# Kernel tuning notes

Hardware: AMD Instinct MI355X
Metric: run time of the kernel (lower is better)

Reference implementation:

```python
import jax, jax.numpy as jnp
import numpy as np

N_NODES = 50000
N_EDGES = 800000
H = 64  # n_hid


def _linear_params(key, fan_in, fan_out):
    lim = 1.0 / np.sqrt(fan_in)
    kw, kb = jax.random.split(key)
    w = jax.random.uniform(kw, (fan_in, fan_out), minval=-lim, maxval=lim, dtype=jnp.float32)
    b = jax.random.uniform(kb, (fan_out,), minval=-lim, maxval=lim, dtype=jnp.float32)
    return w, b


def setup_inputs() -> dict:
    key = jax.random.key(0)
    ks = jax.random.split(key, 10)
    nf_gc = jax.random.normal(ks[0], (N_NODES, H), dtype=jnp.float32)
    src = jax.random.randint(ks[1], (N_EDGES,), 0, N_NODES, dtype=jnp.int32)
    dst = jax.random.randint(ks[2], (N_EDGES,), 0, N_NODES, dtype=jnp.int32)
    res_w1, res_b1 = _linear_params(ks[3], H, H)
    res_w2, res_b2 = _linear_params(ks[4], H, H)
    lin1_w, lin1_b = _linear_params(ks[5], H, H)
    lin2_w, lin2_b = _linear_params(ks[6], H, H)
    msg_w1, msg_b1 = _linear_params(ks[7], 2 * H, 2 * H)
    msg_w2, msg_b2 = _linear_params(ks[8], 2 * H, 2 * H + 1)
    red_w, red_b = _linear_params(ks[9], 3 * H, H)
    return {
        'nf_gc': nf_gc, 'src': src, 'dst': dst,
        'res_w1': res_w1, 'res_b1': res_b1, 'res_w2': res_w2, 'res_b2': res_b2,
        'lin1_w': lin1_w, 'lin1_b': lin1_b, 'lin2_w': lin2_w, 'lin2_b': lin2_b,
        'msg_w1': msg_w1, 'msg_b1': msg_b1, 'msg_w2': msg_w2, 'msg_b2': msg_b2,
        'red_w': red_w, 'red_b': red_b,
    }


def reference(nf_gc, src, dst, res_w1, res_b1, res_w2, res_b2,
              lin1_w, lin1_b, lin2_w, lin2_b,
              msg_w1, msg_b1, msg_w2, msg_b2, red_w, red_b):
    n = nf_gc.shape[0]
    h = lin1_w.shape[0]
    # Residual block: lin2(lin1(x)) + x (no activation)
    x = ((nf_gc @ res_w1 + res_b1) @ res_w2 + res_b2) + nf_gc
    x1 = x @ lin1_w + lin1_b
    # Edge message: concat(src feat, dst feat) -> MLP(2h -> 2h -> 2h+1)
    e = jnp.concatenate([x[src], x[dst]], axis=1)          # [E, 2h]
    hmid = jax.nn.leaky_relu(e @ msg_w1 + msg_b1, 0.2)     # [E, 2h]
    o = hmid @ msg_w2 + msg_b2                             # [E, 2h+1]
    k = jax.nn.sigmoid(o[:, :1])
    f1 = o[:, 1:1 + h] * k
    f2 = o[:, 1 + h:] * k
    # Scatter-reduce: sum for f1, max for f2 (DGL gives 0 for isolated nodes)
    nfoc1 = jax.ops.segment_sum(f1, dst, num_segments=n)
    neg_inf = jnp.array(-jnp.inf, dtype=f2.dtype)
    nfoc2 = jnp.full((n, h), neg_inf, dtype=f2.dtype).at[dst].max(f2)
    deg = jnp.zeros((n,), dtype=f2.dtype).at[dst].add(1.0)
    nfoc2 = jnp.where(deg[:, None] > 0, nfoc2, 0.0)
    # Node reduce MLP (single linear 3h -> h), then outer lin2
    new_x = jnp.concatenate([x, nfoc1, nfoc2], axis=1) @ red_w + red_b
    x2 = new_x @ lin2_w + lin2_b
    return x1 + x2
```

## Files before the change

kernel.cpp:

```cpp
#include <hip/hip_runtime.h>

#define NN 50000
#define NE 800000

typedef _Float16 half8 __attribute__((ext_vector_type(8)));
typedef _Float16 half4 __attribute__((ext_vector_type(4)));
typedef _Float16 half2v __attribute__((ext_vector_type(2)));
typedef float f32x4 __attribute__((ext_vector_type(4)));
typedef unsigned long long u64;

static const size_t XHOFF  = 0;
static const size_t POFF   = 3200000;
static const size_t QOFF   = 6400000;
static const size_t N1OFF  = 9600000;
static const size_t N2OFF  = 12800000;
static const size_t W2TOFF = 16000000;
static const size_t WGHOFF = 16008192;
static const size_t RW1HOFF= 16008256;
static const size_t RW2HOFF= 16010304;
static const size_t L1WHOFF= 16012352;
static const size_t PWHOFF = 16014400;
static const size_t QWHOFF = 16018496;
static const size_t CNTOFF = 16022592;
static const size_t CUROFF = 16072592;
static const size_t PARTOFF= 16122592;
static const size_t SDOFF  = 16122848;
static const size_t FWOFF  = 17722848;
static const size_t FBOFF  = 17729200;

__device__ __forceinline__ unsigned fenc(float f){
  unsigned b = __float_as_uint(f);
  return (b & 0x80000000u) ? ~b : (b | 0x80000000u);
}
__device__ __forceinline__ float fdec(unsigned u){
  return (u & 0x80000000u) ? __uint_as_float(u & 0x7fffffffu) : __uint_as_float(~u);
}

__device__ __forceinline__ int kperm(int kp){
  const int kg = kp >> 5, rem = kp & 31, kt = rem >> 2, j = rem & 3;
  return kt*16 + kg*4 + j;
}

__global__ __launch_bounds__(256) void prep_k(
    const float* __restrict__ w2, const float* __restrict__ rw1,
    const float* __restrict__ rw2, const float* __restrict__ l1w,
    const float* __restrict__ mw1,
    const float* __restrict__ redw, const float* __restrict__ redb,
    const float* __restrict__ l2w, const float* __restrict__ l2b,
    _Float16* __restrict__ w2t, _Float16* __restrict__ w2gh,
    _Float16* __restrict__ rw1h, _Float16* __restrict__ rw2h,
    _Float16* __restrict__ l1wh, _Float16* __restrict__ pwh,
    _Float16* __restrict__ qwh,
    _Float16* __restrict__ fwh, float* __restrict__ fb,
    uint4* __restrict__ nfz,
    const int* __restrict__ dst, unsigned* __restrict__ counts)
{
  __shared__ float sl2[64][8];
  const int b = blockIdx.x;
  if (b < 177){
    int i = b * 256 + threadIdx.x;
    if (i < 16384){
      int c = i >> 7, kp = i & 127;
      w2t[i] = (_Float16)w2[kperm(kp)*129 + 1 + c];
    } else if (i < 16512){
      int kp = i - 16384;
      w2gh[kp] = (_Float16)w2[kperm(kp)*129];
    } else if (i < 20608){
      int idx = i - 16512, c = idx >> 6, k = idx & 63;
      rw1h[idx] = (_Float16)rw1[k*64 + c];
    } else if (i < 24704){
      int idx = i - 20608, c = idx >> 6, k = idx & 63;
      rw2h[idx] = (_Float16)rw2[k*64 + c];
    } else if (i < 28800){
      int idx = i - 24704, c = idx >> 6, k = idx & 63;
      l1wh[idx] = (_Float16)l1w[k*64 + c];
    } else if (i < 36992){
      int idx = i - 28800, c = idx >> 6, k = idx & 63;
      pwh[idx] = (_Float16)mw1[k*128 + c];
    } else if (i < 45184){
      int idx = i - 36992, c = idx >> 6, k = idx & 63;
      qwh[idx] = (_Float16)mw1[(64 + k)*128 + c];
    }
  } else if (b < 185){
    const int b2 = b - 177;
    const int c0 = b2 * 8;
    const int t = threadIdx.x;
    #pragma unroll
    for (int i = 0; i < 2; ++i){
      int idx = t + i*256;
      int j = idx >> 3, cc = idx & 7;
      sl2[j][cc] = l2w[j*64 + c0 + cc];
    }
    __syncthreads();
    for (int o = t; o < 1536; o += 256){
      int k = o >> 3, cc = o & 7;
      const float4* rw = (const float4*)&redw[k*64];
      float a = 0.f;
      #pragma unroll
      for (int q = 0; q < 16; ++q){
        const float4 r4 = rw[q];
        a = fmaf(r4.x, sl2[q*4+0][cc], a);
        a = fmaf(r4.y, sl2[q*4+1][cc], a);
        a = fmaf(r4.z, sl2[q*4+2][cc], a);
        a = fmaf(r4.w, sl2[q*4+3][cc], a);
      }
      fwh[(size_t)(c0 + cc)*192 + k] = (_Float16)a;
    }
    if (t < 8){
      float a = l2b[c0 + t];
      #pragma unroll 8
      for (int j = 0; j < 64; ++j) a = fmaf(redb[j], sl2[j][t], a);
      fb[c0 + t] = a;
    }
  } else if (b < 1748){
    const size_t i0 = ((size_t)(b - 185) * 256 + threadIdx.x) * 4;
    #pragma unroll
    for (int i = 0; i < 4; ++i){
      const size_t idx = i0 + i;
      if (idx < 1600000) nfz[idx] = make_uint4(0u,0u,0u,0u);
    }
  } else {
    int e = (b - 1748) * 256 + threadIdx.x;
    if (e < NE) atomicAdd(&counts[dst[e]], 1u);
  }
}

__global__ __launch_bounds__(256) void scanA(const unsigned* __restrict__ counts,
                                             unsigned* __restrict__ partial)
{
  __shared__ unsigned s[256];
  const int t = threadIdx.x;
  const int idx = blockIdx.x * 256 + t;
  s[t] = (idx < NN) ? counts[idx] : 0u;
  __syncthreads();
  for (int d = 128; d > 0; d >>= 1){
    if (t < d) s[t] += s[t + d];
    __syncthreads();
  }
  if (t == 0) partial[blockIdx.x] = s[0];
}

__global__ __launch_bounds__(256) void scanC2(const unsigned* __restrict__ counts,
                                              const unsigned* __restrict__ partial,
                                              unsigned* __restrict__ cursor)
{
  __shared__ unsigned sp[256];
  __shared__ unsigned s[256];
  const int t = threadIdx.x;
  const int b = blockIdx.x;
  sp[t] = (t < 196 && t < b) ? partial[t] : 0u;
  __syncthreads();
  for (int d = 128; d > 0; d >>= 1){
    if (t < d) sp[t] += sp[t + d];
    __syncthreads();
  }
  const unsigned boff = sp[0];
  const int idx = b * 256 + t;
  unsigned v = (idx < NN) ? counts[idx] : 0u;
  s[t] = v;
  __syncthreads();
  for (int d = 1; d < 256; d <<= 1){
    unsigned u = (t >= d) ? s[t - d] : 0u;
    __syncthreads();
    s[t] += u;
    __syncthreads();
  }
  if (idx < NN) cursor[idx] = boff + s[t] - v;
}

__global__ __launch_bounds__(256) void combo_k(
    const int* __restrict__ src, const int* __restrict__ dst,
    unsigned* __restrict__ cursor, u64* __restrict__ sdbuf,
    const float* __restrict__ nf,
    const _Float16* __restrict__ rw1h, const float* __restrict__ rb1,
    const _Float16* __restrict__ rw2h, const float* __restrict__ rb2,
    const _Float16* __restrict__ l1wh, const float* __restrict__ l1b,
    const _Float16* __restrict__ pwh, const _Float16* __restrict__ qwh,
    const float* __restrict__ mb1,
    _Float16* __restrict__ xh, _Float16* __restrict__ Pp, _Float16* __restrict__ Qp,
    float* __restrict__ out)
{
  __shared__ _Float16 sM[64][72];
  __shared__ _Float16 sT[64][72];
  const int b = blockIdx.x;
  const int t = threadIdx.x;

  if (b < 3125){
    int e = b * 256 + t;
    if (e < NE){
      const int d = dst[e];
      unsigned slot = atomicAdd(&cursor[d], 1u);
      sdbuf[slot] = ((u64)(unsigned)d << 32) | (unsigned)src[e];
    }
    return;
  }

  const int lane = t & 63, wv = t >> 6;
  const int l15 = lane & 15, kg = lane >> 4;
  const int n0 = (b - 3125) * 64;

  {
    const int rr = t >> 4, c4 = (t & 15) * 4;
    #pragma unroll
    for (int i = 0; i < 4; ++i){
      int r = rr + i*16, n = n0 + r;
      float4 v = make_float4(0.f,0.f,0.f,0.f);
      if (n < NN) v = *(const float4*)&nf[(size_t)n*64 + c4];
      half4 h; h[0]=(_Float16)v.x; h[1]=(_Float16)v.y; h[2]=(_Float16)v.z; h[3]=(_Float16)v.w;
      *(half4*)&sM[r][c4] = h;
    }
  }
  __syncthreads();

  const int col = wv*16 + l15;

  {
    half4 bf[4];
    #pragma unroll
    for (int kt = 0; kt < 4; ++kt) bf[kt] = *(const half4*)&rw1h[col*64 + kt*16 + kg*4];
    const float bias = rb1[col];
    #pragma unroll
    for (int rt = 0; rt < 4; ++rt){
      f32x4 acc = {0.f,0.f,0.f,0.f};
      #pragma unroll
      for (int kt = 0; kt < 4; ++kt){
        const half4 af = *(const half4*)&sM[rt*16 + l15][kt*16 + kg*4];
        acc = __builtin_amdgcn_mfma_f32_16x16x16f16(af, bf[kt], acc, 0, 0, 0);
      }
      #pragma unroll
      for (int reg = 0; reg < 4; ++reg)
        sT[rt*16 + kg*4 + reg][col] = (_Float16)(acc[reg] + bias);
    }
  }
  __syncthreads();

  {
    half4 bf[4];
    #pragma unroll
    for (int kt = 0; kt < 4; ++kt) bf[kt] = *(const half4*)&rw2h[col*64 + kt*16 + kg*4];
    const float bias = rb2[col];
    #pragma unroll
    for (int rt = 0; rt < 4; ++rt){
      f32x4 acc = {0.f,0.f,0.f,0.f};
      #pragma unroll
      for (int kt = 0; kt < 4; ++kt){
        const half4 af = *(const half4*)&sT[rt*16 + l15][kt*16 + kg*4];
        acc = __builtin_amdgcn_mfma_f32_16x16x16f16(af, bf[kt], acc, 0, 0, 0);
      }
      #pragma unroll
      for (int reg = 0; reg < 4; ++reg){
        const int row = rt*16 + kg*4 + reg;
        const float xv = acc[reg] + bias + (float)sM[row][col];
        const _Float16 xvh = (_Float16)xv;
        const int n = n0 + row;
        if (n < NN) xh[(size_t)n*64 + col] = xvh;
        sM[row][col] = xvh;
      }
    }
  }
  __syncthreads();

  {
    half4 bf[4];
    #pragma unroll
    for (int kt = 0; kt < 4; ++kt) bf[kt] = *(const half4*)&l1wh[col*64 + kt*16 + kg*4];
    const float bias = l1b[col];
    #pragma unroll
    for (int rt = 0; rt < 4; ++rt){
      f32x4 acc = {0.f,0.f,0.f,0.f};
      #pragma unroll
      for (int kt = 0; kt < 4; ++kt){
        const half4 af = *(const half4*)&sM[rt*16 + l15][kt*16 + kg*4];
        acc = __builtin_amdgcn_mfma_f32_16x16x16f16(af, bf[kt], acc, 0, 0, 0);
      }
      #pragma unroll
      for (int reg = 0; reg < 4; ++reg){
        const int row = rt*16 + kg*4 + reg;
        const int n = n0 + row;
        if (n < NN) out[(size_t)n*64 + col] = acc[reg] + bias;
      }
    }
  }

  #pragma unroll
  for (int g = 0; g < 2; ++g){
    const _Float16* WH = g ? qwh : pwh;
    _Float16* dstp = g ? Qp : Pp;
    #pragma unroll
    for (int h = 0; h < 2; ++h){
      const int ct = h*4 + wv;
      const int colp = ct*16 + l15;
      half4 bf[4];
      #pragma unroll
      for (int kt = 0; kt < 4; ++kt) bf[kt] = *(const half4*)&WH[colp*64 + kt*16 + kg*4];
      const float bias = g ? 0.f : mb1[colp];
      const int kgc = l15 >> 2, jj = l15 & 3;
      const int pos = kgc*32 + ct*4 + jj;
      #pragma unroll
      for (int rt = 0; rt < 4; ++rt){
        f32x4 acc = {0.f,0.f,0.f,0.f};
        #pragma unroll
        for (int kt = 0; kt < 4; ++kt){
          const half4 af = *(const half4*)&sM[rt*16 + l15][kt*16 + kg*4];
          acc = __builtin_amdgcn_mfma_f32_16x16x16f16(af, bf[kt], acc, 0, 0, 0);
        }
        #pragma unroll
        for (int reg = 0; reg < 4; ++reg){
          const int row = rt*16 + kg*4 + reg;
          const int n = n0 + row;
          if (n < NN) dstp[(size_t)n*128 + pos] = (_Float16)(acc[reg] + bias);
        }
      }
    }
  }
}

__global__ __launch_bounds__(256) void edge_mlp11(
    const u64* __restrict__ sd,
    const _Float16* __restrict__ Pp, const _Float16* __restrict__ Qp,
    const _Float16* __restrict__ w2t, const _Float16* __restrict__ w2gh,
    const float* __restrict__ b2,
    float* __restrict__ nfoc1, unsigned* __restrict__ nfoc2)
{
  __shared__ _Float16 sA[64][132];
  __shared__ _Float16 sOutHh[64][68];
  __shared__ float sK[2][64];
  __shared__ int   sD[2][64];
  const int t = threadIdx.x;
  const int lane = t & 63, wv = t >> 6;
  const int r  = lane & 15;
  const int kg = lane >> 4;
  const int row0 = wv * 16;
  const int base = blockIdx.x * 256;

  half4 bf0[8], bf1[8];
  half8 wgr[4];
  float bias0, bias1;
  {
    const int col0 = wv*16 + r, col1 = (wv+4)*16 + r;
    bias0 = b2[1 + col0]; bias1 = b2[1 + col1];
    const _Float16* w0p = &w2t[(size_t)col0*128 + kg*32];
    const _Float16* w1p = &w2t[(size_t)col1*128 + kg*32];
    #pragma unroll
    for (int kt = 0; kt < 8; ++kt){
      bf0[kt] = *(const half4*)&w0p[kt*4];
      bf1[kt] = *(const half4*)&w1p[kt*4];
    }
    #pragma unroll
    for (int i = 0; i < 4; ++i) wgr[i] = *(const half8*)&w2gh[kg*32 + i*8];
  }
  const float gb = b2[0];

#if __has_builtin(__builtin_amdgcn_fdot2)
#define GATE_ACC(MV, WG, GP) { \
    _Pragma("unroll") \
    for (int jj_ = 0; jj_ < 4; ++jj_){ \
      half2v a_ = { MV[jj_*2], MV[jj_*2+1] }; \
      half2v b_ = { WG[jj_*2], WG[jj_*2+1] }; \
      GP = __builtin_amdgcn_fdot2(a_, b_, GP, false); \
    } }
#else
#define GATE_ACC(MV, WG, GP) { \
    _Pragma("unroll") \
    for (int jj_ = 0; jj_ < 8; ++jj_) \
      GP = fmaf((float)MV[jj_], (float)WG[jj_], GP); }
#endif

#define LOADRAW(PH, QH, SS, DD, TILE) { \
    const u64 sdv = sd[base + (TILE)*64 + row0 + r]; \
    SS = (int)(unsigned)(sdv & 0xffffffffu); \
    DD = (int)(unsigned)(sdv >> 32); \
    const _Float16* pr = &Pp[(size_t)SS * 128 + kg*32]; \
    const _Float16* qr = &Qp[(size_t)DD * 128 + kg*32]; \
    PH[0] = *(const half8*)&pr[0];  PH[1] = *(const half8*)&pr[8]; \
    PH[2] = *(const half8*)&pr[16]; PH[3] = *(const half8*)&pr[24]; \
    QH[0] = *(const half8*)&qr[0];  QH[1] = *(const half8*)&qr[8]; \
    QH[2] = *(const half8*)&qr[16]; QH[3] = *(const half8*)&qr[24]; }

#define PROCESS(PH, QH, DD, BUF) { \
    if (kg == 0) sD[BUF][row0 + r] = DD; \
    float gp = 0.f; \
    _Pragma("unroll") \
    for (int i = 0; i < 4; ++i){ \
      half8 mv = PH[i] + QH[i]; \
      const half8 m2 = mv * (_Float16)0.2f; \
      mv = __builtin_elementwise_max(mv, m2); \
      GATE_ACC(mv, wgr[i], gp); \
      *(half8*)&sA[row0 + r][kg*32 + i*8] = mv; \
    } \
    gp += __shfl_xor(gp, 16); \
    gp += __shfl_xor(gp, 32); \
    if (kg == 0) sK[BUF][row0 + r] = 1.f / (1.f + expf(-(gp + gb))); }

#define COMPUTE_HALF(BF, BIAS) { \
    _Pragma("unroll") \
    for (int rt = 0; rt < 4; ++rt){ \
      half4 af[8]; \
      const _Float16* ar = &sA[rt*16 + r][kg*32]; \
      _Pragma("unroll") \
      for (int kt = 0; kt < 8; ++kt) af[kt] = *(const half4*)&ar[kt*4]; \
      f32x4 a0 = {0.f,0.f,0.f,0.f}; \
      _Pragma("unroll") \
      for (int kt = 0; kt < 8; ++kt) \
        a0 = __builtin_amdgcn_mfma_f32_16x16x16f16(af[kt], BF[kt], a0, 0, 0, 0); \
      _Pragma("unroll") \
      for (int reg = 0; reg < 4; ++reg){ \
        const int row = rt*16 + kg*4 + reg; \
        sOutHh[row][wv*16 + r] = (_Float16)(a0[reg] + BIAS); \
      } \
    } }

#define REDUCE_SUM(BUF) { \
    const int c = t & 63; \
    const int rbeg = (t >> 6) * 16; \
    float acc = 0.f; \
    int curd = sD[BUF][rbeg]; \
    _Pragma("unroll 4") \
    for (int rw = rbeg; rw < rbeg + 16; ++rw){ \
      acc += (float)sOutHh[rw][c] * sK[BUF][rw]; \
      const bool last = (rw == rbeg + 15) || (sD[BUF][rw + 1] != curd); \
      if (last){ \
        unsafeAtomicAdd(&nfoc1[(size_t)curd*64 + c], acc); \
        acc = 0.f; \
        if (rw < rbeg + 15) curd = sD[BUF][rw + 1]; \
      } \
    } }

#define REDUCE_MAX(BUF) { \
    const int c = t & 63; \
    const int rbeg = (t >> 6) * 16; \
    float acc = -1e30f; \
    int curd = sD[BUF][rbeg]; \
    _Pragma("unroll 4") \
    for (int rw = rbeg; rw < rbeg + 16; ++rw){ \
      acc = fmaxf(acc, (float)sOutHh[rw][c] * sK[BUF][rw]); \
      const bool last = (rw == rbeg + 15) || (sD[BUF][rw + 1] != curd); \
      if (last){ \
        atomicMax(&nfoc2[(size_t)curd*64 + c], fenc(acc)); \
        acc = -1e30f; \
        if (rw < rbeg + 15) curd = sD[BUF][rw + 1]; \
      } \
    } }

#define TILE_BODY(BUF) \
    __syncthreads(); \
    COMPUTE_HALF(bf0, bias0); \
    __syncthreads(); \
    REDUCE_SUM(BUF); \
    __syncthreads(); \
    COMPUTE_HALF(bf1, bias1); \
    __syncthreads(); \
    REDUCE_MAX(BUF);

  int s0, d0, s1, d1;
  half8 ph0[4], qh0[4], ph1[4], qh1[4];

  LOADRAW(ph0, qh0, s0, d0, 0);

  LOADRAW(ph1, qh1, s1, d1, 1);
  PROCESS(ph0, qh0, d0, 0);
  TILE_BODY(0);

  LOADRAW(ph0, qh0, s0, d0, 2);
  PROCESS(ph1, qh1, d1, 1);
  TILE_BODY(1);

  LOADRAW(ph1, qh1, s1, d1, 3);
  PROCESS(ph0, qh0, d0, 0);
  TILE_BODY(0);

  PROCESS(ph1, qh1, d1, 1);
  TILE_BODY(1);

#undef LOADRAW
#undef PROCESS
#undef COMPUTE_HALF
#undef REDUCE_SUM
#undef REDUCE_MAX
#undef TILE_BODY
#undef GATE_ACC
}

__global__ __launch_bounds__(256) void node_post_m(
    const _Float16* __restrict__ xh, const float* __restrict__ nfoc1,
    const unsigned* __restrict__ nfoc2, const unsigned* __restrict__ counts,
    const _Float16* __restrict__ fwh, const float* __restrict__ fb,
    float* __restrict__ out)
{
  __shared__ _Float16 sC[64][200];
  const int t = threadIdx.x;
  const int lane = t & 63, wv = t >> 6;
  const int l15 = lane & 15, kg = lane >> 4;
  const int n0 = blockIdx.x * 64;

  {
    const int rr = t >> 4, c4 = (t & 15) * 4;
    #pragma unroll
    for (int i = 0; i < 4; ++i){
      int r = rr + i*16, n = n0 + r;
      half4 xv = {};
      float4 f1 = make_float4(0,0,0,0);
      uint4 f2 = make_uint4(0,0,0,0);
      bool has = false;
      if (n < NN){
        xv = *(const half4*)&xh[(size_t)n*64 + c4];
        f1 = *(const float4*)&nfoc1[(size_t)n*64 + c4];
        f2 = *(const uint4*)&nfoc2[(size_t)n*64 + c4];
        has = counts[n] > 0u;
      }
      *(half4*)&sC[r][c4] = xv;
      half4 h1; h1[0]=(_Float16)f1.x; h1[1]=(_Float16)f1.y; h1[2]=(_Float16)f1.z; h1[3]=(_Float16)f1.w;
      *(half4*)&sC[r][64 + c4] = h1;
      half4 h2;
      h2[0] = has ? (_Float16)fdec(f2.x) : (_Float16)0.f;
      h2[1] = has ? (_Float16)fdec(f2.y) : (_Float16)0.f;
      h2[2] = has ? (_Float16)fdec(f2.z) : (_Float16)0.f;
      h2[3] = has ? (_Float16)fdec(f2.w) : (_Float16)0.f;
      *(half4*)&sC[r][128 + c4] = h2;
    }
  }
  __syncthreads();

  const int col = wv*16 + l15;
  half4 bf[12];
  #pragma unroll
  for (int kt = 0; kt < 12; ++kt) bf[kt] = *(const half4*)&fwh[col*192 + kt*16 + kg*4];
  const float bias = fb[col];

  #pragma unroll
  for (int rt = 0; rt < 4; ++rt){
    f32x4 acc = {0.f,0.f,0.f,0.f};
    #pragma unroll
    for (int kt = 0; kt < 12; ++kt){
      const half4 af = *(const half4*)&sC[rt*16 + l15][kt*16 + kg*4];
      acc = __builtin_amdgcn_mfma_f32_16x16x16f16(af, bf[kt], acc, 0, 0, 0);
    }
    #pragma unroll
    for (int reg = 0; reg < 4; ++reg){
      const int row = rt*16 + kg*4 + reg;
      const int n = n0 + row;
      if (n < NN) out[(size_t)n*64 + col] += acc[reg] + bias;
    }
  }
}

extern "C" void kernel_launch(void* const* d_in, const int* in_sizes, int n_in,
                              void* d_out, int out_size, void* d_ws, size_t ws_size,
                              hipStream_t stream)
{
  const float* nf   = (const float*)d_in[0];
  const int*   src  = (const int*)d_in[1];
  const int*   dst  = (const int*)d_in[2];
  const float* rw1  = (const float*)d_in[3];
  const float* rb1  = (const float*)d_in[4];
  const float* rw2  = (const float*)d_in[5];
  const float* rb2  = (const float*)d_in[6];
  const float* l1w  = (const float*)d_in[7];
  const float* l1b  = (const float*)d_in[8];
  const float* l2w  = (const float*)d_in[9];
  const float* l2b  = (const float*)d_in[10];
  const float* mw1  = (const float*)d_in[11];
  const float* mb1  = (const float*)d_in[12];
  const float* mw2  = (const float*)d_in[13];
  const float* mb2  = (const float*)d_in[14];
  const float* redw = (const float*)d_in[15];
  const float* redb = (const float*)d_in[16];

  float* ws = (float*)d_ws;
  _Float16*  xh     = (_Float16*)(ws + XHOFF);
  _Float16*  P      = (_Float16*)(ws + POFF);
  _Float16*  Q      = (_Float16*)(ws + QOFF);
  float*     nfoc1  = ws + N1OFF;
  unsigned*  nfoc2  = (unsigned*)(ws + N2OFF);
  _Float16*  w2t    = (_Float16*)(ws + W2TOFF);
  _Float16*  w2gh   = (_Float16*)(ws + WGHOFF);
  _Float16*  rw1h   = (_Float16*)(ws + RW1HOFF);
  _Float16*  rw2h   = (_Float16*)(ws + RW2HOFF);
  _Float16*  l1wh   = (_Float16*)(ws + L1WHOFF);
  _Float16*  pwh    = (_Float16*)(ws + PWHOFF);
  _Float16*  qwh    = (_Float16*)(ws + QWHOFF);
  unsigned*  counts = (unsigned*)(ws + CNTOFF);
  unsigned*  cursor = (unsigned*)(ws + CUROFF);
  unsigned*  partial= (unsigned*)(ws + PARTOFF);
  u64*       sdbuf  = (u64*)(ws + SDOFF);
  _Float16*  fwh    = (_Float16*)(ws + FWOFF);
  float*     fb     = ws + FBOFF;
  float*     out    = (float*)d_out;

  hipMemsetAsync(counts, 0, NN * sizeof(unsigned), stream);
  hipLaunchKernelGGL(prep_k, dim3(1748 + 3125), dim3(256), 0, stream,
                     mw2, rw1, rw2, l1w, mw1, redw, redb, l2w, l2b,
                     w2t, w2gh, rw1h, rw2h, l1wh, pwh, qwh, fwh, fb,
                     (uint4*)nfoc1, dst, counts);
  hipLaunchKernelGGL(scanA, dim3(196), dim3(256), 0, stream, counts, partial);
  hipLaunchKernelGGL(scanC2, dim3(196), dim3(256), 0, stream, counts, partial, cursor);
  hipLaunchKernelGGL(combo_k, dim3(3125 + 782), dim3(256), 0, stream,
                     src, dst, cursor, sdbuf,
                     nf, rw1h, rb1, rw2h, rb2, l1wh, l1b, pwh, qwh, mb1,
                     xh, P, Q, out);
  hipLaunchKernelGGL(edge_mlp11, dim3(3125), dim3(256), 0, stream,
                     sdbuf, P, Q, w2t, w2gh, mb2, nfoc1, nfoc2);
  hipLaunchKernelGGL(node_post_m, dim3(782), dim3(256), 0, stream,
                     xh, nfoc1, nfoc2, counts, fwh, fb, out);
}
```

Before: 280.8 us.

## Merge scan kernels, move lin1 into node post, use lighter edge barriers

Replaces the two-kernel scan with a single kernel in which each block sums all preceding counts directly, removing one launch. The lin1 projection moves from combo_k into the node post kernel, where its MFMAs run on the x slice already staged in shared memory. This removes the write and read-modify-write of out in fp32. The edge kernel's __syncthreads are replaced by raw s_barrier plus an lgkmcnt wait and sched barriers, to cut barrier overhead. The trade-offs are redundant reads of counts in the scan (later blocks read up to about 50K values) and reliance on the vmcnt not needing a wait at those barriers.

```diff
diff --git a/kernel.cpp b/kernel.cpp
--- a/kernel.cpp
+++ b/kernel.cpp
@@ -23,7 +23,6 @@
 static const size_t QWHOFF = 16018496;
 static const size_t CNTOFF = 16022592;
 static const size_t CUROFF = 16072592;
-static const size_t PARTOFF= 16122592;
 static const size_t SDOFF  = 16122848;
 static const size_t FWOFF  = 17722848;
 static const size_t FBOFF  = 17729200;
@@ -125,30 +124,17 @@
   }
 }
 
-__global__ __launch_bounds__(256) void scanA(const unsigned* __restrict__ counts,
-                                             unsigned* __restrict__ partial)
-{
-  __shared__ unsigned s[256];
-  const int t = threadIdx.x;
-  const int idx = blockIdx.x * 256 + t;
-  s[t] = (idx < NN) ? counts[idx] : 0u;
-  __syncthreads();
-  for (int d = 128; d > 0; d >>= 1){
-    if (t < d) s[t] += s[t + d];
-    __syncthreads();
-  }
-  if (t == 0) partial[blockIdx.x] = s[0];
-}
-
-__global__ __launch_bounds__(256) void scanC2(const unsigned* __restrict__ counts,
-                                              const unsigned* __restrict__ partial,
+__global__ __launch_bounds__(256) void scanAC(const unsigned* __restrict__ counts,
                                               unsigned* __restrict__ cursor)
 {
   __shared__ unsigned sp[256];
   __shared__ unsigned s[256];
   const int t = threadIdx.x;
   const int b = blockIdx.x;
-  sp[t] = (t < 196 && t < b) ? partial[t] : 0u;
+  unsigned acc = 0;
+  const int lim = b * 256;
+  for (int i = t; i < lim; i += 256) acc += counts[i];
+  sp[t] = acc;
   __syncthreads();
   for (int d = 128; d > 0; d >>= 1){
     if (t < d) sp[t] += sp[t + d];
@@ -174,11 +160,9 @@
     const float* __restrict__ nf,
     const _Float16* __restrict__ rw1h, const float* __restrict__ rb1,
     const _Float16* __restrict__ rw2h, const float* __restrict__ rb2,
-    const _Float16* __restrict__ l1wh, const float* __restrict__ l1b,
     const _Float16* __restrict__ pwh, const _Float16* __restrict__ qwh,
     const float* __restrict__ mb1,
-    _Float16* __restrict__ xh, _Float16* __restrict__ Pp, _Float16* __restrict__ Qp,
-    float* __restrict__ out)
+    _Float16* __restrict__ xh, _Float16* __restrict__ Pp, _Float16* __restrict__ Qp)
 {
   __shared__ _Float16 sM[64][72];
   __shared__ _Float16 sT[64][72];
@@ -259,28 +243,6 @@
     }
   }
   __syncthreads();
-
-  {
-    half4 bf[4];
-    #pragma unroll
-    for (int kt = 0; kt < 4; ++kt) bf[kt] = *(const half4*)&l1wh[col*64 + kt*16 + kg*4];
-    const float bias = l1b[col];
-    #pragma unroll
-    for (int rt = 0; rt < 4; ++rt){
-      f32x4 acc = {0.f,0.f,0.f,0.f};
-      #pragma unroll
-      for (int kt = 0; kt < 4; ++kt){
-        const half4 af = *(const half4*)&sM[rt*16 + l15][kt*16 + kg*4];
-        acc = __builtin_amdgcn_mfma_f32_16x16x16f16(af, bf[kt], acc, 0, 0, 0);
-      }
-      #pragma unroll
-      for (int reg = 0; reg < 4; ++reg){
-        const int row = rt*16 + kg*4 + reg;
-        const int n = n0 + row;
-        if (n < NN) out[(size_t)n*64 + col] = acc[reg] + bias;
-      }
-    }
-  }
 
   #pragma unroll
   for (int g = 0; g < 2; ++g){
@@ -315,7 +277,7 @@
   }
 }
 
-__global__ __launch_bounds__(256) void edge_mlp11(
+__global__ __launch_bounds__(256) void edge_mlp12(
     const u64* __restrict__ sd,
     const _Float16* __restrict__ Pp, const _Float16* __restrict__ Qp,
     const _Float16* __restrict__ w2t, const _Float16* __restrict__ w2gh,
@@ -332,6 +294,12 @@
   const int kg = lane >> 4;
   const int row0 = wv * 16;
   const int base = blockIdx.x * 256;
+
+#define SYNC() { \
+    __builtin_amdgcn_sched_barrier(0); \
+    asm volatile("s_waitcnt lgkmcnt(0)" ::: "memory"); \
+    __builtin_amdgcn_s_barrier(); \
+    __builtin_amdgcn_sched_barrier(0); }
 
   half4 bf0[8], bf1[8];
   half8 wgr[4];
@@ -443,13 +411,13 @@
     } }
 
 #define TILE_BODY(BUF) \
-    __syncthreads(); \
+    SYNC(); \
     COMPUTE_HALF(bf0, bias0); \
-    __syncthreads(); \
+    SYNC(); \
     REDUCE_SUM(BUF); \
-    __syncthreads(); \
+    SYNC(); \
     COMPUTE_HALF(bf1, bias1); \
-    __syncthreads(); \
+    SYNC(); \
     REDUCE_MAX(BUF);
 
   int s0, d0, s1, d1;
@@ -479,11 +447,13 @@
 #undef REDUCE_MAX
 #undef TILE_BODY
 #undef GATE_ACC
-}
-
-__global__ __launch_bounds__(256) void node_post_m(
+#undef SYNC
+}
+
+__global__ __launch_bounds__(256) void node_post_m2(
     const _Float16* __restrict__ xh, const float* __restrict__ nfoc1,
     const unsigned* __restrict__ nfoc2, const unsigned* __restrict__ counts,
+    const _Float16* __restrict__ l1wh, const float* __restrict__ l1b,
     const _Float16* __restrict__ fwh, const float* __restrict__ fb,
     float* __restrict__ out)
 {
@@ -522,15 +492,23 @@
   __syncthreads();
 
   const int col = wv*16 + l15;
+  half4 bl[4];
+  #pragma unroll
+  for (int kt = 0; kt < 4; ++kt) bl[kt] = *(const half4*)&l1wh[col*64 + kt*16 + kg*4];
   half4 bf[12];
   #pragma unroll
   for (int kt = 0; kt < 12; ++kt) bf[kt] = *(const half4*)&fwh[col*192 + kt*16 + kg*4];
-  const float bias = fb[col];
+  const float bias = fb[col] + l1b[col];
 
   #pragma unroll
   for (int rt = 0; rt < 4; ++rt){
     f32x4 acc = {0.f,0.f,0.f,0.f};
     #pragma unroll
+    for (int kt = 0; kt < 4; ++kt){
+      const half4 af = *(const half4*)&sC[rt*16 + l15][kt*16 + kg*4];
+      acc = __builtin_amdgcn_mfma_f32_16x16x16f16(af, bl[kt], acc, 0, 0, 0);
+    }
+    #pragma unroll
     for (int kt = 0; kt < 12; ++kt){
       const half4 af = *(const half4*)&sC[rt*16 + l15][kt*16 + kg*4];
       acc = __builtin_amdgcn_mfma_f32_16x16x16f16(af, bf[kt], acc, 0, 0, 0);
@@ -539,7 +517,7 @@
     for (int reg = 0; reg < 4; ++reg){
       const int row = rt*16 + kg*4 + reg;
       const int n = n0 + row;
-      if (n < NN) out[(size_t)n*64 + col] += acc[reg] + bias;
+      if (n < NN) out[(size_t)n*64 + col] = acc[reg] + bias;
     }
   }
 }
@@ -581,7 +559,6 @@
   _Float16*  qwh    = (_Float16*)(ws + QWHOFF);
   unsigned*  counts = (unsigned*)(ws + CNTOFF);
   unsigned*  cursor = (unsigned*)(ws + CUROFF);
-  unsigned*  partial= (unsigned*)(ws + PARTOFF);
   u64*       sdbuf  = (u64*)(ws + SDOFF);
   _Float16*  fwh    = (_Float16*)(ws + FWOFF);
   float*     fb     = ws + FBOFF;
@@ -592,14 +569,12 @@
                      mw2, rw1, rw2, l1w, mw1, redw, redb, l2w, l2b,
                      w2t, w2gh, rw1h, rw2h, l1wh, pwh, qwh, fwh, fb,
                      (uint4*)nfoc1, dst, counts);
-  hipLaunchKernelGGL(scanA, dim3(196), dim3(256), 0, stream, counts, partial);
-  hipLaunchKernelGGL(scanC2, dim3(196), dim3(256), 0, stream, counts, partial, cursor);
+  hipLaunchKernelGGL(scanAC, dim3(196), dim3(256), 0, stream, counts, cursor);
   hipLaunchKernelGGL(combo_k, dim3(3125 + 782), dim3(256), 0, stream,
                      src, dst, cursor, sdbuf,
-                     nf, rw1h, rb1, rw2h, rb2, l1wh, l1b, pwh, qwh, mb1,
-                     xh, P, Q, out);
-  hipLaunchKernelGGL(edge_mlp11, dim3(3125), dim3(256), 0, stream,
+                     nf, rw1h, rb1, rw2h, rb2, pwh, qwh, mb1, xh, P, Q);
+  hipLaunchKernelGGL(edge_mlp12, dim3(3125), dim3(256), 0, stream,
                      sdbuf, P, Q, w2t, w2gh, mb2, nfoc1, nfoc2);
-  hipLaunchKernelGGL(node_post_m, dim3(782), dim3(256), 0, stream,
-                     xh, nfoc1, nfoc2, counts, fwh, fb, out);
-}
+  hipLaunchKernelGGL(node_post_m2, dim3(782), dim3(256), 0, stream,
+                     xh, nfoc1, nfoc2, counts, l1wh, l1b, fwh, fb, out);
+}
```

Measured after the change: 302.8 us. 7.8% more time.
